# Performance work log

Measured on AMD Instinct MI355X. Metric: run time of the kernel, lower is better.

The kernel has to match this reference:

```python
import jax, jax.numpy as jnp
import numpy as np

N = 50000      # nodes per node type
E = 800000     # edges per meta-step (avg degree 16)
DIN = 16       # input feature dim (all node types)
DMSG = 16      # dim_message per meta-step
F = 16         # edge feature dim
DOUT = 32      # dim_out of final linear


def setup_inputs() -> dict:
    key = jax.random.key(0)
    ks = jax.random.split(key, 17)
    s = 0.1  # param scale
    return {
        "x_indivi": jax.random.normal(ks[0], (N, DIN), jnp.float32),
        "x_src_a": jax.random.normal(ks[1], (N, DIN), jnp.float32),
        "x_src_b": jax.random.normal(ks[2], (N, DIN), jnp.float32),
        "edge_index_a": jax.random.randint(ks[3], (2, E), 0, N),
        "edge_index_b": jax.random.randint(ks[4], (2, E), 0, N),
        "edge_attr_a": jax.random.normal(ks[5], (E, F), jnp.float32),
        "edge_attr_b": jax.random.normal(ks[6], (E, F), jnp.float32),
        # message_function of NNConv: Linear(F, DIN*DMSG), stored as [F, DIN, DMSG]
        "w_msg_a": jax.random.normal(ks[7], (F, DIN, DMSG), jnp.float32) * s,
        "b_msg_a": jax.random.normal(ks[8], (DIN, DMSG), jnp.float32) * s,
        "root_a": jax.random.normal(ks[9], (DIN, DMSG), jnp.float32) * s,
        "bias_a": jax.random.normal(ks[10], (DMSG,), jnp.float32) * s,
        "w_msg_b": jax.random.normal(ks[11], (F, DIN, DMSG), jnp.float32) * s,
        "b_msg_b": jax.random.normal(ks[12], (DIN, DMSG), jnp.float32) * s,
        "root_b": jax.random.normal(ks[13], (DIN, DMSG), jnp.float32) * s,
        "bias_b": jax.random.normal(ks[14], (DMSG,), jnp.float32) * s,
        # final linear: Linear(2*DMSG, DOUT), stored as [2*DMSG, DOUT]
        "w_lin": jax.random.normal(ks[15], (2 * DMSG, DOUT), jnp.float32) * s,
        "b_lin": jax.random.normal(ks[16], (DOUT,), jnp.float32) * s,
    }


def _nnconv(x_src, x_dst, edge_index, edge_attr, w_msg, b_msg, root, bias):
    """PyG NNConv with sum aggregation.
    W_e = edge_attr @ w_msg + b_msg  (per-edge [DIN, DMSG] weight matrix)
    msg_e = x_src[src_e] @ W_e ; out = segment_sum(msg) + x_dst @ root + bias
    """
    src, dst = edge_index[0], edge_index[1]
    xj = x_src[src]  # [E, DIN] gather
    # fused per-edge bmm: einsum contracts without keeping W_e longer than needed
    msg = jnp.einsum('ef,fio,ei->eo', edge_attr, w_msg, xj) + xj @ b_msg  # [E, DMSG]
    agg = jax.ops.segment_sum(msg, dst, num_segments=x_dst.shape[0])  # scatter-add
    return agg + x_dst @ root + bias


def reference(x_indivi, x_src_a, x_src_b, edge_index_a, edge_index_b,
              edge_attr_a, edge_attr_b,
              w_msg_a, b_msg_a, root_a, bias_a,
              w_msg_b, b_msg_b, root_b, bias_b,
              w_lin, b_lin):
    msg_a = jax.nn.sigmoid(_nnconv(x_src_a, x_indivi, edge_index_a, edge_attr_a,
                                   w_msg_a, b_msg_a, root_a, bias_a))
    msg_b = jax.nn.sigmoid(_nnconv(x_src_b, x_indivi, edge_index_b, edge_attr_b,
                                   w_msg_b, b_msg_b, root_b, bias_b))
    msg_cat = jnp.concatenate([msg_a, msg_b], axis=1)  # [N, 2*DMSG]
    return jax.nn.sigmoid(msg_cat @ w_lin + b_lin)     # [N, DOUT]
```

## Files before the change

### kernel.cpp

```cpp
#include <hip/hip_runtime.h>
#include <hip/hip_bf16.h>
#include <stdint.h>


#define NN 50000
#define EE 800000

typedef __attribute__((ext_vector_type(8))) short short8;
typedef __attribute__((ext_vector_type(4))) float f32x4;

union U8 { short8 v; unsigned int u[4]; };

__device__ __forceinline__ unsigned short f2bf_rne(float f) {
    union { float fl; unsigned int i; } v; v.fl = f;
    unsigned int x = v.i;
    x += 0x7FFFu + ((x >> 16) & 1u);
    return (unsigned short)(x >> 16);
}

__device__ __forceinline__ unsigned int pack2bf(float a, float b) {
    __hip_bfloat162 h = __float22bfloat162_rn(float2{a, b});
    union { __hip_bfloat162 h2; unsigned int u; } c; c.h2 = h;
    return c.u;
}

__global__ void prep_w(const float* __restrict__ w_msg_a, const float* __restrict__ b_msg_a,
                       unsigned short* __restrict__ wf_a,
                       const float* __restrict__ w_msg_b, const float* __restrict__ b_msg_b,
                       unsigned short* __restrict__ wf_b) {
    const float* w_msg = blockIdx.x ? w_msg_b : w_msg_a;
    const float* b_msg = blockIdx.x ? b_msg_b : b_msg_a;
    unsigned short* wfrag = blockIdx.x ? wf_b : wf_a;
    for (int idx = threadIdx.x; idx < 9 * 64 * 8; idx += 256) {
        int j = idx & 7;
        int lane = (idx >> 3) & 63;
        int t = idx >> 9;
        int k = 32 * t + (lane >> 4) * 8 + j;
        int n = lane & 15;
        int f = k >> 4, i = k & 15;
        float v = (f < 16) ? w_msg[f * 256 + i * 16 + n]
                           : (f == 16 ? b_msg[i * 16 + n] : 0.f);
        wfrag[idx] = f2bf_rne(v);
    }
}

__global__ __launch_bounds__(256) void edge_mfma(
    const int* __restrict__ ei_a, const float* __restrict__ ea_a,
    const float* __restrict__ x_a, const unsigned short* __restrict__ wf_a,
    float* __restrict__ agg_a,
    const int* __restrict__ ei_b, const float* __restrict__ ea_b,
    const float* __restrict__ x_b, const unsigned short* __restrict__ wf_b,
    float* __restrict__ agg_b)
{
    int ms = blockIdx.x & 1;
    const int* __restrict__ eidx  = ms ? ei_b : ei_a;
    const float* __restrict__ attr = ms ? ea_b : ea_a;
    const float* __restrict__ x    = ms ? x_b : x_a;
    const unsigned short* __restrict__ wfrag = ms ? wf_b : wf_a;
    float* __restrict__ agg = ms ? agg_b : agg_a;

    int lane = threadIdx.x & 63;
    int m = lane & 15, quad = lane >> 4;
    int q2 = quad >> 1, qb = quad & 1;
    int wave = ((blockIdx.x >> 1) * 256 + (int)threadIdx.x) >> 6;
    int nwaves = (gridDim.x >> 1) * 4;

    short8 bfr[9];
    #pragma unroll
    for (int t = 0; t < 9; ++t)
        bfr[t] = ((const short8*)wfrag)[t * 64 + lane];

    for (int g = wave; g < EE / 16; g += nwaves) {
        int ebase = g * 16;
        int src = eidx[ebase + m];
        int dstr[4];
        #pragma unroll
        for (int r = 0; r < 4; ++r)
            dstr[r] = eidx[EE + ebase + quad * 4 + r];

        const float4* xr = (const float4*)(x + (size_t)src * 16);
        float4 x0 = xr[qb * 2];
        float4 x1 = xr[qb * 2 + 1];
        float xh[8] = {x0.x, x0.y, x0.z, x0.w, x1.x, x1.y, x1.z, x1.w};

        const float* ar = attr + (size_t)(ebase + m) * 16;
        float ah[8];
        #pragma unroll
        for (int t = 0; t < 8; ++t) ah[t] = ar[2 * t + q2];

        f32x4 acc = {0.f, 0.f, 0.f, 0.f};
        #pragma unroll
        for (int t = 0; t < 8; ++t) {
            U8 a;
            #pragma unroll
            for (int jj = 0; jj < 4; ++jj)
                a.u[jj] = pack2bf(ah[t] * xh[2 * jj], ah[t] * xh[2 * jj + 1]);
            acc = __builtin_amdgcn_mfma_f32_16x16x32_bf16(a.v, bfr[t], acc, 0, 0, 0);
        }
        U8 a8;
        #pragma unroll
        for (int jj = 0; jj < 4; ++jj)
            a8.u[jj] = (q2 == 0) ? pack2bf(xh[2 * jj], xh[2 * jj + 1]) : 0u;
        acc = __builtin_amdgcn_mfma_f32_16x16x32_bf16(a8.v, bfr[8], acc, 0, 0, 0);

        #pragma unroll
        for (int r = 0; r < 4; ++r)
            atomicAdd(&agg[dstr[r] * 16 + m], acc[r]);
    }
}

__global__ __launch_bounds__(256) void finalize(
    const float* __restrict__ xind,
    const float* __restrict__ agg_a, const float* __restrict__ agg_b,
    const float* __restrict__ root_a, const float* __restrict__ bias_a,
    const float* __restrict__ root_b, const float* __restrict__ bias_b,
    const float* __restrict__ w_lin, const float* __restrict__ b_lin,
    float* __restrict__ out)
{
    int tid = threadIdx.x;
    int n = blockIdx.x * 8 + (tid >> 5);
    if (n >= NN) return;
    int d = tid & 31;
    int lane = tid & 63;
    int gb32 = lane & ~31;

    float xv = xind[n * 16 + (d & 15)];

    int j = d & 15;
    const float* root = (d < 16) ? root_a : root_b;
    const float* bias = (d < 16) ? bias_a : bias_b;
    const float* agg  = (d < 16) ? agg_a  : agg_b;

    float acc = agg[n * 16 + j] + bias[j];
    #pragma unroll
    for (int i = 0; i < 16; ++i) {
        float xiv = __shfl(xv, gb32 + i);
        acc += xiv * root[i * 16 + j];
    }
    float h = 1.f / (1.f + __expf(-acc));

    float acc2 = b_lin[d];
    #pragma unroll
    for (int jj = 0; jj < 32; ++jj) {
        float hj = __shfl(h, gb32 + jj);
        acc2 += hj * w_lin[jj * 32 + d];
    }
    out[(size_t)n * 32 + d] = 1.f / (1.f + __expf(-acc2));
}

extern "C" void kernel_launch(void* const* d_in, const int* in_sizes, int n_in,
                              void* d_out, int out_size, void* d_ws, size_t ws_size,
                              hipStream_t stream) {
    (void)in_sizes; (void)n_in; (void)out_size; (void)ws_size;
    const float* x_indivi = (const float*)d_in[0];
    const float* x_src_a  = (const float*)d_in[1];
    const float* x_src_b  = (const float*)d_in[2];
    const int*   ei_a     = (const int*)d_in[3];
    const int*   ei_b     = (const int*)d_in[4];
    const float* ea_a     = (const float*)d_in[5];
    const float* ea_b     = (const float*)d_in[6];
    const float* w_msg_a  = (const float*)d_in[7];
    const float* b_msg_a  = (const float*)d_in[8];
    const float* root_a   = (const float*)d_in[9];
    const float* bias_a   = (const float*)d_in[10];
    const float* w_msg_b  = (const float*)d_in[11];
    const float* b_msg_b  = (const float*)d_in[12];
    const float* root_b   = (const float*)d_in[13];
    const float* bias_b   = (const float*)d_in[14];
    const float* w_lin    = (const float*)d_in[15];
    const float* b_lin    = (const float*)d_in[16];
    float* out = (float*)d_out;

    char* ws = (char*)d_ws;
    size_t off = 0;
    unsigned short* wf_a = (unsigned short*)(ws + off); off += 9 * 64 * 8 * 2;
    unsigned short* wf_b = (unsigned short*)(ws + off); off += 9 * 64 * 8 * 2;
    float* agg_a = (float*)(ws + off); off += (size_t)NN * 16 * 4;
    float* agg_b = (float*)(ws + off); off += (size_t)NN * 16 * 4;

    hipMemsetAsync(agg_a, 0, (size_t)NN * 16 * 4 * 2, stream);
    prep_w<<<2, 256, 0, stream>>>(w_msg_a, b_msg_a, wf_a, w_msg_b, b_msg_b, wf_b);

    edge_mfma<<<2048, 256, 0, stream>>>(ei_a, ea_a, x_src_a, wf_a, agg_a,
                                        ei_b, ea_b, x_src_b, wf_b, agg_b);

    finalize<<<(NN + 7) / 8, 256, 0, stream>>>(
        x_indivi, agg_a, agg_b, root_a, bias_a, root_b, bias_b, w_lin, b_lin, out);
}
```

Baseline: 286.4 us.

## Bucket edges by destination block and aggregate in LDS instead of global atomics

Adds a bucketing pass that groups edges by destination-node block of 32 nodes using per-bucket atomic counters. The edge kernel then processes one bucket per workgroup, accumulates messages with LDS atomics, and writes each node's aggregate once, removing the global atomics and the aggregate memset. The edge-attribute loads become float4 gathers by edge id, with the weight fragment layout reordered to match. The cost is an extra pass doing 1.6M global atomics, gathered (non-coalesced) attribute and index reads, and a fixed bucket capacity that silently drops edges if a bucket overflows.

```diff
diff --git a/kernel.cpp b/kernel.cpp
--- a/kernel.cpp
+++ b/kernel.cpp
@@ -5,6 +5,8 @@
 
 #define NN 50000
 #define EE 800000
+#define NPB 32
+#define NB 1563
 
 typedef __attribute__((ext_vector_type(8))) short short8;
 typedef __attribute__((ext_vector_type(4))) float f32x4;
@@ -35,13 +37,31 @@
         int j = idx & 7;
         int lane = (idx >> 3) & 63;
         int t = idx >> 9;
-        int k = 32 * t + (lane >> 4) * 8 + j;
         int n = lane & 15;
-        int f = k >> 4, i = k & 15;
+        int qb = (lane >> 4) & 1;
+        int q2 = (lane >> 5) & 1;
+        int i = qb * 8 + j;
+        int f = (t < 8) ? (8 * q2 + t) : (16 + q2);
         float v = (f < 16) ? w_msg[f * 256 + i * 16 + n]
                            : (f == 16 ? b_msg[i * 16 + n] : 0.f);
         wfrag[idx] = f2bf_rne(v);
     }
+}
+
+__global__ __launch_bounds__(256) void bucket_scatter(
+    const int* __restrict__ ei_a, const int* __restrict__ ei_b,
+    unsigned int* __restrict__ cnt, int* __restrict__ col, int cap)
+{
+    int idx = blockIdx.x * 256 + threadIdx.x;
+    if (idx >= 2 * EE) return;
+    int ms = idx >= EE;
+    int e = ms ? idx - EE : idx;
+    const int* ei = ms ? ei_b : ei_a;
+    int dst = ei[EE + e];
+    int b = dst >> 5;
+    unsigned int p = atomicAdd(&cnt[ms * NB + b], 1u);
+    if (p < (unsigned int)cap)
+        col[(size_t)(ms * NB + b) * cap + p] = e;
 }
 
 __global__ __launch_bounds__(256) void edge_mfma(
@@ -50,43 +70,55 @@
     float* __restrict__ agg_a,
     const int* __restrict__ ei_b, const float* __restrict__ ea_b,
     const float* __restrict__ x_b, const unsigned short* __restrict__ wf_b,
-    float* __restrict__ agg_b)
+    float* __restrict__ agg_b,
+    const unsigned int* __restrict__ cnt, const int* __restrict__ col, int cap)
 {
     int ms = blockIdx.x & 1;
-    const int* __restrict__ eidx  = ms ? ei_b : ei_a;
+    int b  = blockIdx.x >> 1;
+    const int* __restrict__ ei     = ms ? ei_b : ei_a;
     const float* __restrict__ attr = ms ? ea_b : ea_a;
     const float* __restrict__ x    = ms ? x_b : x_a;
     const unsigned short* __restrict__ wfrag = ms ? wf_b : wf_a;
     float* __restrict__ agg = ms ? agg_b : agg_a;
 
-    int lane = threadIdx.x & 63;
+    __shared__ float agg_lds[NPB * 16];
+    int tid = threadIdx.x;
+    agg_lds[tid] = 0.f;
+    agg_lds[tid + 256] = 0.f;
+    __syncthreads();
+
+    int lane = tid & 63, wid = tid >> 6;
     int m = lane & 15, quad = lane >> 4;
     int q2 = quad >> 1, qb = quad & 1;
-    int wave = ((blockIdx.x >> 1) * 256 + (int)threadIdx.x) >> 6;
-    int nwaves = (gridDim.x >> 1) * 4;
 
     short8 bfr[9];
     #pragma unroll
     for (int t = 0; t < 9; ++t)
         bfr[t] = ((const short8*)wfrag)[t * 64 + lane];
 
-    for (int g = wave; g < EE / 16; g += nwaves) {
-        int ebase = g * 16;
-        int src = eidx[ebase + m];
-        int dstr[4];
-        #pragma unroll
-        for (int r = 0; r < 4; ++r)
-            dstr[r] = eidx[EE + ebase + quad * 4 + r];
+    int cntb = (int)cnt[ms * NB + b];
+    if (cntb > cap) cntb = cap;
+    const int* __restrict__ colb = col + (size_t)(ms * NB + b) * cap;
+    int nb0 = b * NPB;
+
+    for (int c = wid; c * 16 < cntb; c += 4) {
+        int base = c * 16;
+        bool vm = (base + m) < cntb;
+        int e = vm ? colb[base + m] : 0;
+        int src = ei[e];
+        int de  = ei[EE + e];
 
         const float4* xr = (const float4*)(x + (size_t)src * 16);
         float4 x0 = xr[qb * 2];
         float4 x1 = xr[qb * 2 + 1];
-        float xh[8] = {x0.x, x0.y, x0.z, x0.w, x1.x, x1.y, x1.z, x1.w};
-
-        const float* ar = attr + (size_t)(ebase + m) * 16;
-        float ah[8];
-        #pragma unroll
-        for (int t = 0; t < 8; ++t) ah[t] = ar[2 * t + q2];
+        float zf = vm ? 1.f : 0.f;
+        float xh[8] = {x0.x * zf, x0.y * zf, x0.z * zf, x0.w * zf,
+                       x1.x * zf, x1.y * zf, x1.z * zf, x1.w * zf};
+
+        const float4* ar = (const float4*)(attr + (size_t)e * 16);
+        float4 a0 = ar[q2 * 2];
+        float4 a1 = ar[q2 * 2 + 1];
+        float ah[8] = {a0.x, a0.y, a0.z, a0.w, a1.x, a1.y, a1.z, a1.w};
 
         f32x4 acc = {0.f, 0.f, 0.f, 0.f};
         #pragma unroll
@@ -104,9 +136,19 @@
         acc = __builtin_amdgcn_mfma_f32_16x16x32_bf16(a8.v, bfr[8], acc, 0, 0, 0);
 
         #pragma unroll
-        for (int r = 0; r < 4; ++r)
-            atomicAdd(&agg[dstr[r] * 16 + m], acc[r]);
-    }
+        for (int r = 0; r < 4; ++r) {
+            int slot = base + quad * 4 + r;
+            int d = __shfl(de, quad * 4 + r);
+            if (slot < cntb)
+                atomicAdd(&agg_lds[(d - nb0) * 16 + m], acc[r]);
+        }
+    }
+    __syncthreads();
+
+    int i0 = tid, i1 = tid + 256;
+    int n0 = nb0 + (i0 >> 4), n1 = nb0 + (i1 >> 4);
+    if (n0 < NN) agg[(size_t)n0 * 16 + (i0 & 15)] = agg_lds[i0];
+    if (n1 < NN) agg[(size_t)n1 * 16 + (i1 & 15)] = agg_lds[i1];
 }
 
 __global__ __launch_bounds__(256) void finalize(
@@ -151,7 +193,7 @@
 extern "C" void kernel_launch(void* const* d_in, const int* in_sizes, int n_in,
                               void* d_out, int out_size, void* d_ws, size_t ws_size,
                               hipStream_t stream) {
-    (void)in_sizes; (void)n_in; (void)out_size; (void)ws_size;
+    (void)in_sizes; (void)n_in; (void)out_size;
     const float* x_indivi = (const float*)d_in[0];
     const float* x_src_a  = (const float*)d_in[1];
     const float* x_src_b  = (const float*)d_in[2];
@@ -173,16 +215,29 @@
 
     char* ws = (char*)d_ws;
     size_t off = 0;
-    unsigned short* wf_a = (unsigned short*)(ws + off); off += 9 * 64 * 8 * 2;
-    unsigned short* wf_b = (unsigned short*)(ws + off); off += 9 * 64 * 8 * 2;
-    float* agg_a = (float*)(ws + off); off += (size_t)NN * 16 * 4;
-    float* agg_b = (float*)(ws + off); off += (size_t)NN * 16 * 4;
-
-    hipMemsetAsync(agg_a, 0, (size_t)NN * 16 * 4 * 2, stream);
+    auto alloc = [&](size_t bytes) -> void* {
+        void* p = ws + off;
+        off += (bytes + 255) & ~(size_t)255;
+        return p;
+    };
+    unsigned short* wf_a = (unsigned short*)alloc(9 * 64 * 8 * 2);
+    unsigned short* wf_b = (unsigned short*)alloc(9 * 64 * 8 * 2);
+    unsigned int*   cnt  = (unsigned int*)alloc(2 * NB * 4);
+    float* agg_a = (float*)alloc((size_t)NN * 16 * 4);
+    float* agg_b = (float*)alloc((size_t)NN * 16 * 4);
+    size_t avail = ws_size > off ? ws_size - off : 0;
+    int cap = (int)(avail / (2 * (size_t)NB * 4));
+    if (cap > 1024) cap = 1024;
+    int* col = (int*)(ws + off);
+
+    hipMemsetAsync(cnt, 0, 2 * NB * 4, stream);
     prep_w<<<2, 256, 0, stream>>>(w_msg_a, b_msg_a, wf_a, w_msg_b, b_msg_b, wf_b);
 
-    edge_mfma<<<2048, 256, 0, stream>>>(ei_a, ea_a, x_src_a, wf_a, agg_a,
-                                        ei_b, ea_b, x_src_b, wf_b, agg_b);
+    bucket_scatter<<<(2 * EE + 255) / 256, 256, 0, stream>>>(ei_a, ei_b, cnt, col, cap);
+
+    edge_mfma<<<2 * NB, 256, 0, stream>>>(ei_a, ea_a, x_src_a, wf_a, agg_a,
+                                          ei_b, ea_b, x_src_b, wf_b, agg_b,
+                                          cnt, col, cap);
 
     finalize<<<(NN + 7) / 8, 256, 0, stream>>>(
         x_indivi, agg_a, agg_b, root_a, bias_a, root_b, bias_b, w_lin, b_lin, out);
```

New measurement: 542.8 us. 89.5% more time.
